# Performance work log

Hardware: AMD Instinct MI355X
Metric: run time of the kernel (lower is better)

The kernel has to match this reference:

```python
import jax, jax.numpy as jnp
import numpy as np
import math

N_EMBED = 768
N_HEAD = 12
BLOCK_SIZE = 2048
B, T = 4, 2048


def setup_inputs() -> dict:
    key = jax.random.key(0)
    ks = jax.random.split(key, 5)
    x = jax.random.normal(ks[0], (B, T, N_EMBED), dtype=jnp.float32)
    # attn: Linear(n_embed, 3*n_embed); torch Linear stores W as [out,in]
    s = 1.0 / math.sqrt(N_EMBED)
    W_attn = jax.random.uniform(ks[1], (3 * N_EMBED, N_EMBED), minval=-s, maxval=s, dtype=jnp.float32)
    b_attn = jax.random.uniform(ks[2], (3 * N_EMBED,), minval=-s, maxval=s, dtype=jnp.float32)
    W_o = jax.random.uniform(ks[3], (N_EMBED, N_EMBED), minval=-s, maxval=s, dtype=jnp.float32)
    b_o = jax.random.uniform(ks[4], (N_EMBED,), minval=-s, maxval=s, dtype=jnp.float32)
    return {"x": x, "W_attn": W_attn, "b_attn": b_attn, "W_o": W_o, "b_o": b_o}


def reference(x, W_attn, b_attn, W_o, b_o):
    Bsz, Tlen, C = x.shape
    hd = C // N_HEAD
    qkv = x @ W_attn.T + b_attn                       # [B,T,3C]
    q, k, v = jnp.split(qkv, 3, axis=2)
    # [B,H,T,hd]
    q = q.reshape(Bsz, Tlen, N_HEAD, hd).transpose(0, 2, 1, 3)
    k = k.reshape(Bsz, Tlen, N_HEAD, hd).transpose(0, 2, 1, 3)
    v = v.reshape(Bsz, Tlen, N_HEAD, hd).transpose(0, 2, 1, 3)
    att = jnp.einsum('bhqd,bhkd->bhqk', q, k) * (1.0 / math.sqrt(hd))
    causal = jnp.tril(jnp.ones((Tlen, Tlen), dtype=bool))
    att = jnp.where(causal[None, None], att, -jnp.inf)
    att = jax.nn.softmax(att, axis=-1)
    y = jnp.einsum('bhqk,bhkd->bhqd', att, v)          # [B,H,T,hd]
    y = y.transpose(0, 2, 1, 3).reshape(Bsz, Tlen, C)
    return y @ W_o.T + b_o
```

## Files before the change

### kernel.cpp

```cpp
#include <hip/hip_runtime.h>

#define H 12
#define T 2048
#define HD 64
#define CEMB 768
#define M1 8192
#define N1 2304
#define K1 768

typedef __attribute__((ext_vector_type(8))) short bf8;
typedef __attribute__((ext_vector_type(4))) float f4;
typedef __attribute__((ext_vector_type(16))) float f16v;
typedef __attribute__((ext_vector_type(4))) int i4;

__device__ __forceinline__ unsigned short f2bf(float f){
  union { float f; unsigned u; } v; v.f = f;
  unsigned r = v.u + 0x7FFFu + ((v.u >> 16) & 1u);
  return (unsigned short)(r >> 16);
}

__device__ __forceinline__ int cvtpk(float a, float b){
  int r;
  asm("v_cvt_pk_bf16_f32 %0, %1, %2" : "=v"(r) : "v"(a), "v"(b));
  return r;
}

__device__ __forceinline__ void gload16(const unsigned short* g, unsigned short* l){
  __builtin_amdgcn_global_load_lds((const __attribute__((address_space(1))) void*)g,
                                   (__attribute__((address_space(3))) void*)l, 16, 0, 0);
}

__global__ __launch_bounds__(256) void cvt_all(const float* __restrict__ x,
                                               const float* __restrict__ wa,
                                               const float* __restrict__ wo,
                                               unsigned short* __restrict__ xb,
                                               unsigned short* __restrict__ wab,
                                               unsigned short* __restrict__ wob){
  const int n4x = M1 * K1 / 4, n4a = N1 * K1 / 4, n4o = CEMB * CEMB / 4;
  int i = blockIdx.x * blockDim.x + threadIdx.x;
  const float* in; unsigned short* out; int j;
  if (i < n4x){ in = x; out = xb; j = i; }
  else if (i < n4x + n4a){ in = wa; out = wab; j = i - n4x; }
  else if (i < n4x + n4a + n4o){ in = wo; out = wob; j = i - n4x - n4a; }
  else return;
  float4 v = ((const float4*)in)[j];
  ushort4 o;
  o.x = f2bf(v.x); o.y = f2bf(v.y); o.z = f2bf(v.z); o.w = f2bf(v.w);
  ((ushort4*)out)[j] = o;
}

__global__ __launch_bounds__(256) void gemm_qkv(const unsigned short* __restrict__ A,
                                                const unsigned short* __restrict__ Wb,
                                                const float* __restrict__ bias,
                                                unsigned short* __restrict__ Qb,
                                                unsigned short* __restrict__ Kb,
                                                unsigned short* __restrict__ Vr){
  __shared__ __align__(16) unsigned short As[128][64];
  __shared__ __align__(16) unsigned short Bs[128][64];
  int Lid = blockIdx.x + gridDim.x * blockIdx.y;
  int L2 = (Lid & 7) * 144 + (Lid >> 3);
  const int m0 = (L2 / 18) * 128, n0 = (L2 % 18) * 128;
  const int tid = threadIdx.x, w = tid >> 6, lane = tid & 63;
  const int wm = (w >> 1) * 64, wn = (w & 1) * 64;
  const int l15 = lane & 15, g = lane >> 4;
  const int srow = lane >> 3;
  const int scol = ((lane & 7) ^ srow) * 8;
  f4 acc[4][4] = {};
  for (int k0 = 0; k0 < K1; k0 += 64){
    #pragma unroll
    for (int i = 0; i < 4; ++i){
      int rb = i * 32 + w * 8;
      gload16(&A [(size_t)(m0 + rb + srow) * K1 + k0 + scol], &As[rb][0]);
      gload16(&Wb[(size_t)(n0 + rb + srow) * K1 + k0 + scol], &Bs[rb][0]);
    }
    __syncthreads();
    #pragma unroll
    for (int kq = 0; kq < 2; ++kq){
      bf8 a[4], b[4];
      #pragma unroll
      for (int i = 0; i < 4; ++i){
        int row = wm + i * 16 + l15;
        a[i] = *(const bf8*)&As[row][(((kq << 2) + g) ^ (row & 7)) * 8];
      }
      #pragma unroll
      for (int j = 0; j < 4; ++j){
        int row = wn + j * 16 + l15;
        b[j] = *(const bf8*)&Bs[row][(((kq << 2) + g) ^ (row & 7)) * 8];
      }
      #pragma unroll
      for (int i = 0; i < 4; ++i)
        #pragma unroll
        for (int j = 0; j < 4; ++j)
          acc[i][j] = __builtin_amdgcn_mfma_f32_16x16x32_bf16(a[i], b[j], acc[i][j], 0, 0, 0);
    }
    __syncthreads();
  }
  #pragma unroll
  for (int j = 0; j < 4; ++j){
    int ncol = n0 + wn + j * 16 + l15;
    float bv = bias[ncol];
    int which = ncol / CEMB;
    int cc = ncol - which * CEMB;
    int h = cc >> 6, d = cc & 63;
    #pragma unroll
    for (int i = 0; i < 4; ++i){
      #pragma unroll
      for (int r = 0; r < 4; ++r){
        int m = m0 + wm + i * 16 + g * 4 + r;
        int b_ = m >> 11, t = m & 2047;
        size_t idx = ((size_t)(b_ * H + h) * T + t) * HD + d;
        float v = acc[i][j][r] + bv;
        if (which == 0)      Qb[idx] = f2bf(v * 0.18033688f);
        else if (which == 1) Kb[idx] = f2bf(v);
        else                 Vr[idx] = f2bf(v);
      }
    }
  }
}

__global__ __launch_bounds__(256) void transpose_v(const unsigned short* __restrict__ Vr,
                                                   unsigned short* __restrict__ Vt){
  __shared__ unsigned short Lb[64][66];
  const int bh = blockIdx.y, tt = blockIdx.x;
  const unsigned short* src = Vr + ((size_t)bh * T + tt * 64) * HD;
  unsigned short* dst = Vt + (size_t)bh * HD * T + tt * 64;
  const int tid = threadIdx.x;
  {
    int r = tid >> 2, c = (tid & 3) * 16;
    uint4 v0 = *(const uint4*)&src[r * HD + c];
    uint4 v1 = *(const uint4*)&src[r * HD + c + 8];
    unsigned* lp = (unsigned*)&Lb[r][c];
    lp[0] = v0.x; lp[1] = v0.y; lp[2] = v0.z; lp[3] = v0.w;
    lp[4] = v1.x; lp[5] = v1.y; lp[6] = v1.z; lp[7] = v1.w;
  }
  __syncthreads();
  {
    int d = tid >> 2, tq = tid & 3;
    unsigned ov[8];
    #pragma unroll
    for (int jj = 0; jj < 8; ++jj){
      unsigned lo = Lb[tq * 16 + 2 * jj][d];
      unsigned hi = Lb[tq * 16 + 2 * jj + 1][d];
      ov[jj] = lo | (hi << 16);
    }
    uint4* op = (uint4*)&dst[(size_t)d * T + tq * 16];
    op[0] = make_uint4(ov[0], ov[1], ov[4], ov[5]);
    op[1] = make_uint4(ov[2], ov[3], ov[6], ov[7]);
  }
}

__global__ __launch_bounds__(64) void attn(const unsigned short* __restrict__ Qb,
                                           const unsigned short* __restrict__ Kb,
                                           const unsigned short* __restrict__ Vt,
                                           unsigned short* __restrict__ Yb){
  __shared__ __align__(16) unsigned short Ks[2][32][64];
  __shared__ __align__(16) unsigned short Vs[2][64][32];
  const int bh = blockIdx.x;
  const int qidx = 63 - (int)blockIdx.y;
  const int lane = threadIdx.x;
  const int q31 = lane & 31, hi = lane >> 5;
  const int q0 = qidx * 32;
  const unsigned short* Qp = Qb + (size_t)bh * T * HD;
  const unsigned short* Kp = Kb + (size_t)bh * T * HD;
  const unsigned short* Vp = Vt + (size_t)bh * HD * T;
  const int b_ = bh / H, h = bh % H;

  const int krow = lane >> 3;
  const int kcs  = ((lane & 7) ^ krow) * 8;
  const int vrow = lane >> 2;
  const int vcs  = ((lane & 3) ^ ((lane >> 4) & 3)) * 8;

  bf8 qf[4];
  #pragma unroll
  for (int ds = 0; ds < 4; ++ds)
    qf[ds] = *(const bf8*)&Qp[(q0 + q31) * HD + ds * 16 + hi * 8];

  bf8 ones;
  #pragma unroll
  for (int j = 0; j < 8; ++j) ones[j] = (short)0x3F80;

  f16v o0 = {}, o1 = {}, ol = {};
  float m_i = -1e30f;
  const int ntw = qidx + 1;

  #pragma unroll
  for (int it = 0; it < 4; ++it)
    gload16(&Kp[(size_t)(it * 8 + krow) * HD + kcs], &Ks[0][it * 8][0]);
  #pragma unroll
  for (int it = 0; it < 4; ++it)
    gload16(&Vp[(size_t)(it * 16 + vrow) * T + vcs], &Vs[0][it * 16][0]);

  #pragma unroll 2
  for (int t = 0; t < ntw; ++t){
    const int cur = t & 1;
    const int kv0 = t * 32;
    if (t + 1 < ntw){
      const int nkv = kv0 + 32;
      #pragma unroll
      for (int it = 0; it < 4; ++it)
        gload16(&Kp[(size_t)(nkv + it * 8 + krow) * HD + kcs], &Ks[cur ^ 1][it * 8][0]);
      #pragma unroll
      for (int it = 0; it < 4; ++it)
        gload16(&Vp[(size_t)(it * 16 + vrow) * T + nkv + vcs], &Vs[cur ^ 1][it * 16][0]);
      asm volatile("s_waitcnt vmcnt(8)" ::: "memory");
    } else {
      asm volatile("s_waitcnt vmcnt(0)" ::: "memory");
    }
    __builtin_amdgcn_sched_barrier(0);

    f16v s0 = {};
    __builtin_amdgcn_s_setprio(1);
    #pragma unroll
    for (int ds = 0; ds < 4; ++ds){
      bf8 k0 = *(const bf8*)&Ks[cur][q31][(((2 * ds + hi)) ^ (q31 & 7)) * 8];
      s0 = __builtin_amdgcn_mfma_f32_32x32x16_bf16(k0, qf[ds], s0, 0, 0, 0);
    }
    __builtin_amdgcn_s_setprio(0);
    if (t == ntw - 1){
      #pragma unroll
      for (int r = 0; r < 16; ++r){
        int kvr = kv0 + (r & 3) + 8 * (r >> 2) + 4 * hi;
        if (kvr > q0 + q31) s0[r] = -1e30f;
      }
    }
    float a0 = fmaxf(fmaxf(s0[0], s0[1]), s0[2]);
    float a1 = fmaxf(fmaxf(s0[3], s0[4]), s0[5]);
    float a2 = fmaxf(fmaxf(s0[6], s0[7]), s0[8]);
    float a3 = fmaxf(fmaxf(s0[9], s0[10]), s0[11]);
    float a4 = fmaxf(fmaxf(s0[12], s0[13]), s0[14]);
    float mx = fmaxf(fmaxf(fmaxf(a0, a1), a2), fmaxf(fmaxf(a3, a4), s0[15]));
    mx = fmaxf(mx, __shfl_xor(mx, 32));
    if (__any(mx > m_i + 8.f)){
      float mn = fmaxf(m_i, mx);
      float sc_ = __builtin_exp2f(m_i - mn);
      #pragma unroll
      for (int r = 0; r < 16; ++r){
        float s = __shfl(sc_, (r & 3) + 8 * (r >> 2) + 4 * hi);
        o0[r] *= s; o1[r] *= s; ol[r] *= s;
      }
      m_i = mn;
    }
    #pragma unroll
    for (int r = 0; r < 16; ++r) s0[r] = __builtin_exp2f(s0[r] - m_i);
    union { i4 i; bf8 h; } pa;
    __builtin_amdgcn_s_setprio(1);
    #pragma unroll
    for (int ks = 0; ks < 2; ++ks){
      const int off = ks * 8;
      pa.i = (i4){ cvtpk(s0[off], s0[off+1]), cvtpk(s0[off+2], s0[off+3]),
                   cvtpk(s0[off+4], s0[off+5]), cvtpk(s0[off+6], s0[off+7]) };
      bf8 v0 = *(const bf8*)&Vs[cur][q31]     [((2 * ks + hi) ^ ((q31 >> 2) & 3)) * 8];
      bf8 v1 = *(const bf8*)&Vs[cur][32 + q31][((2 * ks + hi) ^ ((q31 >> 2) & 3)) * 8];
      o0 = __builtin_amdgcn_mfma_f32_32x32x16_bf16(pa.h, v0, o0, 0, 0, 0);
      o1 = __builtin_amdgcn_mfma_f32_32x32x16_bf16(pa.h, v1, o1, 0, 0, 0);
      ol = __builtin_amdgcn_mfma_f32_32x32x16_bf16(pa.h, ones, ol, 0, 0, 0);
    }
    __builtin_amdgcn_s_setprio(0);
  }

  #pragma unroll
  for (int r = 0; r < 16; ++r){
    int qrow = q0 + (r & 3) + 8 * (r >> 2) + 4 * hi;
    float inv = 1.0f / ol[r];
    size_t base = ((size_t)b_ * T + qrow) * CEMB + h * HD;
    Yb[base + q31]      = f2bf(o0[r] * inv);
    Yb[base + 32 + q31] = f2bf(o1[r] * inv);
  }
}

__global__ __launch_bounds__(256) void gemm_out(const unsigned short* __restrict__ A,
                                                const unsigned short* __restrict__ Wb,
                                                const float* __restrict__ bias,
                                                float* __restrict__ out){
  __shared__ __align__(16) unsigned short As[128][64];
  __shared__ __align__(16) unsigned short Bs[128][64];
  int Lid = blockIdx.x + gridDim.x * blockIdx.y;
  int L2 = (Lid & 7) * 48 + (Lid >> 3);
  const int m0 = (L2 / 6) * 128, n0 = (L2 % 6) * 128;
  const int tid = threadIdx.x, w = tid >> 6, lane = tid & 63;
  const int wm = (w >> 1) * 64, wn = (w & 1) * 64;
  const int l15 = lane & 15, g = lane >> 4;
  const int srow = lane >> 3;
  const int scol = ((lane & 7) ^ srow) * 8;
  f4 acc[4][4] = {};
  for (int k0 = 0; k0 < CEMB; k0 += 64){
    #pragma unroll
    for (int i = 0; i < 4; ++i){
      int rb = i * 32 + w * 8;
      gload16(&A [(size_t)(m0 + rb + srow) * CEMB + k0 + scol], &As[rb][0]);
      gload16(&Wb[(size_t)(n0 + rb + srow) * CEMB + k0 + scol], &Bs[rb][0]);
    }
    __syncthreads();
    #pragma unroll
    for (int kq = 0; kq < 2; ++kq){
      bf8 a[4], b[4];
      #pragma unroll
      for (int i = 0; i < 4; ++i){
        int row = wm + i * 16 + l15;
        a[i] = *(const bf8*)&As[row][(((kq << 2) + g) ^ (row & 7)) * 8];
      }
      #pragma unroll
      for (int j = 0; j < 4; ++j){
        int row = wn + j * 16 + l15;
        b[j] = *(const bf8*)&Bs[row][(((kq << 2) + g) ^ (row & 7)) * 8];
      }
      #pragma unroll
      for (int i = 0; i < 4; ++i)
        #pragma unroll
        for (int j = 0; j < 4; ++j)
          acc[i][j] = __builtin_amdgcn_mfma_f32_16x16x32_bf16(a[i], b[j], acc[i][j], 0, 0, 0);
    }
    __syncthreads();
  }
  #pragma unroll
  for (int j = 0; j < 4; ++j){
    int ncol = n0 + wn + j * 16 + l15;
    float bv = bias[ncol];
    #pragma unroll
    for (int i = 0; i < 4; ++i){
      #pragma unroll
      for (int r = 0; r < 4; ++r){
        int m = m0 + wm + i * 16 + g * 4 + r;
        out[(size_t)m * CEMB + ncol] = acc[i][j][r] + bv;
      }
    }
  }
}

extern "C" void kernel_launch(void* const* d_in, const int* in_sizes, int n_in,
                              void* d_out, int out_size, void* d_ws, size_t ws_size,
                              hipStream_t stream){
  const float* x      = (const float*)d_in[0];
  const float* W_attn = (const float*)d_in[1];
  const float* b_attn = (const float*)d_in[2];
  const float* W_o    = (const float*)d_in[3];
  const float* b_o    = (const float*)d_in[4];
  float* out = (float*)d_out;

  char* ws = (char*)d_ws;
  const size_t SZ_T  = (size_t)48 * T * HD * 2;
  const size_t SZ_WA = (size_t)N1 * K1 * 2;
  const size_t SZ_WO = (size_t)CEMB * CEMB * 2;
  unsigned short* Xb = (unsigned short*)(ws);
  unsigned short* Vt = (unsigned short*)(ws);
  unsigned short* Wa = (unsigned short*)(ws + SZ_T);
  unsigned short* Wo = (unsigned short*)(ws + SZ_T + SZ_WA);
  unsigned short* Qb = (unsigned short*)(ws + SZ_T + SZ_WA + SZ_WO);
  unsigned short* Kb = (unsigned short*)(ws + SZ_T + SZ_WA + SZ_WO + SZ_T);
  unsigned short* Vr = (unsigned short*)(ws + SZ_T + SZ_WA + SZ_WO + 2 * SZ_T);
  unsigned short* Yb = Vr;

  const int n4tot = (M1 * K1 + N1 * K1 + CEMB * CEMB) / 4;
  cvt_all<<<(n4tot + 255) / 256, 256, 0, stream>>>(x, W_attn, W_o, Xb, Wa, Wo);

  gemm_qkv<<<dim3(N1 / 128, M1 / 128), 256, 0, stream>>>(Xb, Wa, b_attn, Qb, Kb, Vr);
  transpose_v<<<dim3(T / 64, 48), 256, 0, stream>>>(Vr, Vt);
  attn<<<dim3(48, 64), 64, 0, stream>>>(Qb, Kb, Vt, Yb);
  gemm_out<<<dim3(CEMB / 128, M1 / 128), 256, 0, stream>>>(Yb, Wo, b_o, out);
}
```

Measured before the change: 168.9 us.

## Pair short and long causal query tiles per attention block for balanced work

Each attention workgroup now processes two 32-row query tiles, j and 63-j, so every block does the same amount of causal work, and the grid is halved. During the shared prefix of key tiles, each K/V tile loaded into LDS is reused by both query tiles, which cuts K/V traffic and LDS reads per query. The cost is roughly doubled accumulator registers, which may lower occupancy, plus fewer total workgroups (1536) to fill the GPU.

```diff
diff --git a/kernel.cpp b/kernel.cpp
--- a/kernel.cpp
+++ b/kernel.cpp
@@ -156,10 +156,11 @@
   __shared__ __align__(16) unsigned short Ks[2][32][64];
   __shared__ __align__(16) unsigned short Vs[2][64][32];
   const int bh = blockIdx.x;
-  const int qidx = 63 - (int)blockIdx.y;
+  const int j = (int)blockIdx.y;
+  const int qa = j, qb = 63 - j;
   const int lane = threadIdx.x;
   const int q31 = lane & 31, hi = lane >> 5;
-  const int q0 = qidx * 32;
+  const int q0a = qa * 32, q0b = qb * 32;
   const unsigned short* Qp = Qb + (size_t)bh * T * HD;
   const unsigned short* Kp = Kb + (size_t)bh * T * HD;
   const unsigned short* Vp = Vt + (size_t)bh * HD * T;
@@ -170,18 +171,20 @@
   const int vrow = lane >> 2;
   const int vcs  = ((lane & 3) ^ ((lane >> 4) & 3)) * 8;
 
-  bf8 qf[4];
-  #pragma unroll
-  for (int ds = 0; ds < 4; ++ds)
-    qf[ds] = *(const bf8*)&Qp[(q0 + q31) * HD + ds * 16 + hi * 8];
+  bf8 qfa[4], qfb[4];
+  #pragma unroll
+  for (int ds = 0; ds < 4; ++ds){
+    qfa[ds] = *(const bf8*)&Qp[(q0a + q31) * HD + ds * 16 + hi * 8];
+    qfb[ds] = *(const bf8*)&Qp[(q0b + q31) * HD + ds * 16 + hi * 8];
+  }
 
   bf8 ones;
   #pragma unroll
-  for (int j = 0; j < 8; ++j) ones[j] = (short)0x3F80;
-
-  f16v o0 = {}, o1 = {}, ol = {};
-  float m_i = -1e30f;
-  const int ntw = qidx + 1;
+  for (int jj = 0; jj < 8; ++jj) ones[jj] = (short)0x3F80;
+
+  f16v o0a = {}, o1a = {}, ola = {};
+  f16v o0b = {}, o1b = {}, olb = {};
+  float m_a = -1e30f, m_b = -1e30f;
 
   #pragma unroll
   for (int it = 0; it < 4; ++it)
@@ -190,11 +193,104 @@
   for (int it = 0; it < 4; ++it)
     gload16(&Vp[(size_t)(it * 16 + vrow) * T + vcs], &Vs[0][it * 16][0]);
 
-  #pragma unroll 2
-  for (int t = 0; t < ntw; ++t){
+  for (int t = 0; t <= qa; ++t){
     const int cur = t & 1;
     const int kv0 = t * 32;
-    if (t + 1 < ntw){
+    {
+      const int nkv = kv0 + 32;
+      #pragma unroll
+      for (int it = 0; it < 4; ++it)
+        gload16(&Kp[(size_t)(nkv + it * 8 + krow) * HD + kcs], &Ks[cur ^ 1][it * 8][0]);
+      #pragma unroll
+      for (int it = 0; it < 4; ++it)
+        gload16(&Vp[(size_t)(it * 16 + vrow) * T + nkv + vcs], &Vs[cur ^ 1][it * 16][0]);
+      asm volatile("s_waitcnt vmcnt(8)" ::: "memory");
+    }
+    __builtin_amdgcn_sched_barrier(0);
+
+    f16v s0a = {}, s0b = {};
+    __builtin_amdgcn_s_setprio(1);
+    #pragma unroll
+    for (int ds = 0; ds < 4; ++ds){
+      bf8 kk = *(const bf8*)&Ks[cur][q31][(((2 * ds + hi)) ^ (q31 & 7)) * 8];
+      s0a = __builtin_amdgcn_mfma_f32_32x32x16_bf16(kk, qfa[ds], s0a, 0, 0, 0);
+      s0b = __builtin_amdgcn_mfma_f32_32x32x16_bf16(kk, qfb[ds], s0b, 0, 0, 0);
+    }
+    __builtin_amdgcn_s_setprio(0);
+    if (t == qa){
+      #pragma unroll
+      for (int r = 0; r < 16; ++r){
+        int kvr = kv0 + (r & 3) + 8 * (r >> 2) + 4 * hi;
+        if (kvr > q0a + q31) s0a[r] = -1e30f;
+      }
+    }
+    {
+      float a0 = fmaxf(fmaxf(s0a[0], s0a[1]), s0a[2]);
+      float a1 = fmaxf(fmaxf(s0a[3], s0a[4]), s0a[5]);
+      float a2 = fmaxf(fmaxf(s0a[6], s0a[7]), s0a[8]);
+      float a3 = fmaxf(fmaxf(s0a[9], s0a[10]), s0a[11]);
+      float a4 = fmaxf(fmaxf(s0a[12], s0a[13]), s0a[14]);
+      float mx = fmaxf(fmaxf(fmaxf(a0, a1), a2), fmaxf(fmaxf(a3, a4), s0a[15]));
+      mx = fmaxf(mx, __shfl_xor(mx, 32));
+      if (__any(mx > m_a + 8.f)){
+        float mn = fmaxf(m_a, mx);
+        float sc_ = __builtin_exp2f(m_a - mn);
+        #pragma unroll
+        for (int r = 0; r < 16; ++r){
+          float s = __shfl(sc_, (r & 3) + 8 * (r >> 2) + 4 * hi);
+          o0a[r] *= s; o1a[r] *= s; ola[r] *= s;
+        }
+        m_a = mn;
+      }
+      #pragma unroll
+      for (int r = 0; r < 16; ++r) s0a[r] = __builtin_exp2f(s0a[r] - m_a);
+    }
+    {
+      float a0 = fmaxf(fmaxf(s0b[0], s0b[1]), s0b[2]);
+      float a1 = fmaxf(fmaxf(s0b[3], s0b[4]), s0b[5]);
+      float a2 = fmaxf(fmaxf(s0b[6], s0b[7]), s0b[8]);
+      float a3 = fmaxf(fmaxf(s0b[9], s0b[10]), s0b[11]);
+      float a4 = fmaxf(fmaxf(s0b[12], s0b[13]), s0b[14]);
+      float mx = fmaxf(fmaxf(fmaxf(a0, a1), a2), fmaxf(fmaxf(a3, a4), s0b[15]));
+      mx = fmaxf(mx, __shfl_xor(mx, 32));
+      if (__any(mx > m_b + 8.f)){
+        float mn = fmaxf(m_b, mx);
+        float sc_ = __builtin_exp2f(m_b - mn);
+        #pragma unroll
+        for (int r = 0; r < 16; ++r){
+          float s = __shfl(sc_, (r & 3) + 8 * (r >> 2) + 4 * hi);
+          o0b[r] *= s; o1b[r] *= s; olb[r] *= s;
+        }
+        m_b = mn;
+      }
+      #pragma unroll
+      for (int r = 0; r < 16; ++r) s0b[r] = __builtin_exp2f(s0b[r] - m_b);
+    }
+    union { i4 i; bf8 h; } paa, pab;
+    __builtin_amdgcn_s_setprio(1);
+    #pragma unroll
+    for (int ks = 0; ks < 2; ++ks){
+      const int off = ks * 8;
+      paa.i = (i4){ cvtpk(s0a[off], s0a[off+1]), cvtpk(s0a[off+2], s0a[off+3]),
+                    cvtpk(s0a[off+4], s0a[off+5]), cvtpk(s0a[off+6], s0a[off+7]) };
+      pab.i = (i4){ cvtpk(s0b[off], s0b[off+1]), cvtpk(s0b[off+2], s0b[off+3]),
+                    cvtpk(s0b[off+4], s0b[off+5]), cvtpk(s0b[off+6], s0b[off+7]) };
+      bf8 v0 = *(const bf8*)&Vs[cur][q31]     [((2 * ks + hi) ^ ((q31 >> 2) & 3)) * 8];
+      bf8 v1 = *(const bf8*)&Vs[cur][32 + q31][((2 * ks + hi) ^ ((q31 >> 2) & 3)) * 8];
+      o0a = __builtin_amdgcn_mfma_f32_32x32x16_bf16(paa.h, v0, o0a, 0, 0, 0);
+      o0b = __builtin_amdgcn_mfma_f32_32x32x16_bf16(pab.h, v0, o0b, 0, 0, 0);
+      o1a = __builtin_amdgcn_mfma_f32_32x32x16_bf16(paa.h, v1, o1a, 0, 0, 0);
+      o1b = __builtin_amdgcn_mfma_f32_32x32x16_bf16(pab.h, v1, o1b, 0, 0, 0);
+      ola = __builtin_amdgcn_mfma_f32_32x32x16_bf16(paa.h, ones, ola, 0, 0, 0);
+      olb = __builtin_amdgcn_mfma_f32_32x32x16_bf16(pab.h, ones, olb, 0, 0, 0);
+    }
+    __builtin_amdgcn_s_setprio(0);
+  }
+
+  for (int t = qa + 1; t <= qb; ++t){
+    const int cur = t & 1;
+    const int kv0 = t * 32;
+    if (t < qb){
       const int nkv = kv0 + 32;
       #pragma unroll
       for (int it = 0; it < 4; ++it)
@@ -212,15 +308,15 @@
     __builtin_amdgcn_s_setprio(1);
     #pragma unroll
     for (int ds = 0; ds < 4; ++ds){
-      bf8 k0 = *(const bf8*)&Ks[cur][q31][(((2 * ds + hi)) ^ (q31 & 7)) * 8];
-      s0 = __builtin_amdgcn_mfma_f32_32x32x16_bf16(k0, qf[ds], s0, 0, 0, 0);
+      bf8 kk = *(const bf8*)&Ks[cur][q31][(((2 * ds + hi)) ^ (q31 & 7)) * 8];
+      s0 = __builtin_amdgcn_mfma_f32_32x32x16_bf16(kk, qfb[ds], s0, 0, 0, 0);
     }
     __builtin_amdgcn_s_setprio(0);
-    if (t == ntw - 1){
+    if (t == qb){
       #pragma unroll
       for (int r = 0; r < 16; ++r){
         int kvr = kv0 + (r & 3) + 8 * (r >> 2) + 4 * hi;
-        if (kvr > q0 + q31) s0[r] = -1e30f;
+        if (kvr > q0b + q31) s0[r] = -1e30f;
       }
     }
     float a0 = fmaxf(fmaxf(s0[0], s0[1]), s0[2]);
@@ -230,18 +326,18 @@
     float a4 = fmaxf(fmaxf(s0[12], s0[13]), s0[14]);
     float mx = fmaxf(fmaxf(fmaxf(a0, a1), a2), fmaxf(fmaxf(a3, a4), s0[15]));
     mx = fmaxf(mx, __shfl_xor(mx, 32));
-    if (__any(mx > m_i + 8.f)){
-      float mn = fmaxf(m_i, mx);
-      float sc_ = __builtin_exp2f(m_i - mn);
+    if (__any(mx > m_b + 8.f)){
+      float mn = fmaxf(m_b, mx);
+      float sc_ = __builtin_exp2f(m_b - mn);
       #pragma unroll
       for (int r = 0; r < 16; ++r){
         float s = __shfl(sc_, (r & 3) + 8 * (r >> 2) + 4 * hi);
-        o0[r] *= s; o1[r] *= s; ol[r] *= s;
-      }
-      m_i = mn;
-    }
-    #pragma unroll
-    for (int r = 0; r < 16; ++r) s0[r] = __builtin_exp2f(s0[r] - m_i);
+        o0b[r] *= s; o1b[r] *= s; olb[r] *= s;
+      }
+      m_b = mn;
+    }
+    #pragma unroll
+    for (int r = 0; r < 16; ++r) s0[r] = __builtin_exp2f(s0[r] - m_b);
     union { i4 i; bf8 h; } pa;
     __builtin_amdgcn_s_setprio(1);
     #pragma unroll
@@ -251,20 +347,24 @@
                    cvtpk(s0[off+4], s0[off+5]), cvtpk(s0[off+6], s0[off+7]) };
       bf8 v0 = *(const bf8*)&Vs[cur][q31]     [((2 * ks + hi) ^ ((q31 >> 2) & 3)) * 8];
       bf8 v1 = *(const bf8*)&Vs[cur][32 + q31][((2 * ks + hi) ^ ((q31 >> 2) & 3)) * 8];
-      o0 = __builtin_amdgcn_mfma_f32_32x32x16_bf16(pa.h, v0, o0, 0, 0, 0);
-      o1 = __builtin_amdgcn_mfma_f32_32x32x16_bf16(pa.h, v1, o1, 0, 0, 0);
-      ol = __builtin_amdgcn_mfma_f32_32x32x16_bf16(pa.h, ones, ol, 0, 0, 0);
+      o0b = __builtin_amdgcn_mfma_f32_32x32x16_bf16(pa.h, v0, o0b, 0, 0, 0);
+      o1b = __builtin_amdgcn_mfma_f32_32x32x16_bf16(pa.h, v1, o1b, 0, 0, 0);
+      olb = __builtin_amdgcn_mfma_f32_32x32x16_bf16(pa.h, ones, olb, 0, 0, 0);
     }
     __builtin_amdgcn_s_setprio(0);
   }
 
   #pragma unroll
   for (int r = 0; r < 16; ++r){
-    int qrow = q0 + (r & 3) + 8 * (r >> 2) + 4 * hi;
-    float inv = 1.0f / ol[r];
-    size_t base = ((size_t)b_ * T + qrow) * CEMB + h * HD;
-    Yb[base + q31]      = f2bf(o0[r] * inv);
-    Yb[base + 32 + q31] = f2bf(o1[r] * inv);
+    int rr = (r & 3) + 8 * (r >> 2) + 4 * hi;
+    float inva = 1.0f / ola[r];
+    size_t basea = ((size_t)b_ * T + q0a + rr) * CEMB + h * HD;
+    Yb[basea + q31]      = f2bf(o0a[r] * inva);
+    Yb[basea + 32 + q31] = f2bf(o1a[r] * inva);
+    float invb = 1.0f / olb[r];
+    size_t baseb = ((size_t)b_ * T + q0b + rr) * CEMB + h * HD;
+    Yb[baseb + q31]      = f2bf(o0b[r] * invb);
+    Yb[baseb + 32 + q31] = f2bf(o1b[r] * invb);
   }
 }
 
@@ -355,6 +455,6 @@
 
   gemm_qkv<<<dim3(N1 / 128, M1 / 128), 256, 0, stream>>>(Xb, Wa, b_attn, Qb, Kb, Vr);
   transpose_v<<<dim3(T / 64, 48), 256, 0, stream>>>(Vr, Vt);
-  attn<<<dim3(48, 64), 64, 0, stream>>>(Qb, Kb, Vt, Yb);
+  attn<<<dim3(48, 32), 64, 0, stream>>>(Qb, Kb, Vt, Yb);
   gemm_out<<<dim3(CEMB / 128, M1 / 128), 256, 0, stream>>>(Yb, Wo, b_o, out);
 }
```

Result: slower. 211.0 us (+24.9%).
